# Optimization experiments

Hardware: AMD Instinct MI355X
Metric: run time of the kernel (lower is better)

## Reference

```python
import jax, jax.numpy as jnp
import numpy as np
import math

G0, G1 = 24, 24           # initial/current grid size (command(initial_grid_size=(24,24), ...))
N = G0 * G1               # 576 spatial tokens
PREFIX = 1                # num_prefix_tokens (cls token)
EPS = 0.1                 # get_eps((24,24)): 0.5*23^2/0.1^2 = 26450 <= 32500, no doubling
COEF = float(max(G0, G1) ** 2)          # 576.0, sigmoid_fn coefficient
B_SHIFT = math.log(COEF - 1.0)          # b = log(575)
CLAMP = max(-0.5 * (max(G0, G1) - 1) ** 2, -6550.0)  # -264.5


def setup_inputs() -> dict:
    key = jax.random.key(0)
    k1, k2, k3 = jax.random.split(key, 3)
    head_dim = 64
    q = jax.random.normal(k1, (8, 12, N + PREFIX, head_dim), dtype=jnp.float32)
    W_var = jax.random.normal(k2, (head_dim, 2), dtype=jnp.float32) * (head_dim ** -0.5)
    b_var = jnp.zeros((2,), dtype=jnp.float32)
    W_alpha = jax.random.normal(k3, (head_dim, 1), dtype=jnp.float32) * (head_dim ** -0.5)
    b_alpha = jnp.zeros((1,), dtype=jnp.float32)
    return {"q": q, "W_var": W_var, "b_var": b_var, "W_alpha": W_alpha, "b_alpha": b_alpha}


def _gaussian_numerator():
    # coords: (N, 2) integer grid positions
    ii, jj = jnp.meshgrid(jnp.arange(G0), jnp.arange(G1), indexing="ij")
    coords = jnp.stack([ii, jj], axis=-1).reshape(N, 2).astype(jnp.float32)
    d = -0.5 * (coords[:, None, :] - coords[None, :, :]) ** 2  # (N, N, 2)
    return jnp.maximum(d, CLAMP)


def reference(q, W_var, b_var, W_alpha, b_alpha):
    qs = q[..., PREFIX:, :]                                   # (B, H, N, C)
    # var = coef * sigmoid(linear(q) - b), shape (B, H, N, 2)
    var = COEF * jax.nn.sigmoid(jnp.einsum("bhnc,ck->bhnk", qs, W_var) + b_var - B_SHIFT)
    # alpha = softplus(linear(q)), shape (B, H, N, 1)
    alpha = jax.nn.softplus(jnp.einsum("bhnc,ck->bhnk", qs, W_alpha) + b_alpha)
    d = _gaussian_numerator()                                 # (N, N, 2)
    # broadcast divide -> sum over coord dim -> exp: (B, H, N, N)
    gaussian = jnp.exp(jnp.sum(d[None, None] / (var[:, :, :, None, :] + EPS), axis=-1))
    addition = alpha * gaussian                               # alpha broadcasts over last dim
    # pad prefix rows/cols with 0 at the beginning -> (B, H, N+1, N+1)
    return jnp.pad(addition, ((0, 0), (0, 0), (PREFIX, 0), (PREFIX, 0)))
```

## Files before the change

kernel.cpp:

```cpp
#include <hip/hip_runtime.h>
#include <math.h>

#define G 24
#define NPTS (G * G)
#define ROWS (NPTS + 1)
#define HD 64
#define BH (8 * 12)
#define EPSF 0.1f
#define COEFF 576.0f
#define BSHIFT 6.3543700408f
#define RPB 8
#define BPI ((ROWS + RPB - 1) / RPB)

typedef float f32x4 __attribute__((ext_vector_type(4)));

__global__ __launch_bounds__(256) void gaussian_augment_kernel(
    const float* __restrict__ q,
    const float* __restrict__ Wv,
    const float* __restrict__ bv,
    const float* __restrict__ Wa,
    const float* __restrict__ ba,
    float* __restrict__ out)
{
    const int bh  = blockIdx.x / BPI;
    const int blk = blockIdx.x - bh * BPI;
    const int r0  = blk * RPB;
    const int Ract = min(RPB, ROWS - r0);
    const int tid = threadIdx.x;

    __shared__ float s_dot[RPB][3];
    __shared__ float s_par[RPB][3];
    __shared__ float s_ex0[RPB][G];
    __shared__ float s_ex1[RPB][G];

    const int wave = tid >> 6;
    const int lane = tid & 63;
    #pragma unroll
    for (int pass = 0; pass < 2; ++pass) {
        const int rr = wave + 4 * pass;
        if (rr < Ract) {
            const int r = r0 + rr;
            const float* qrow = q + ((size_t)bh * ROWS + r) * HD;
            const float qv = qrow[lane];
            float p0 = qv * Wv[2 * lane + 0];
            float p1 = qv * Wv[2 * lane + 1];
            float p2 = qv * Wa[lane];
            #pragma unroll
            for (int off = 32; off >= 1; off >>= 1) {
                p0 += __shfl_xor(p0, off);
                p1 += __shfl_xor(p1, off);
                p2 += __shfl_xor(p2, off);
            }
            if (lane == 0) {
                s_dot[rr][0] = p0;
                s_dot[rr][1] = p1;
                s_dot[rr][2] = p2;
            }
        }
    }
    __syncthreads();

    if (tid < Ract) {
        const int r = r0 + tid;
        const float x0 = s_dot[tid][0] + bv[0] - BSHIFT;
        const float x1 = s_dot[tid][1] + bv[1] - BSHIFT;
        const float xa = s_dot[tid][2] + ba[0];
        const float var0 = COEFF / (1.0f + expf(-x0));
        const float var1 = COEFF / (1.0f + expf(-x1));
        s_par[tid][0] = 1.0f / (var0 + EPSF);
        s_par[tid][1] = 1.0f / (var1 + EPSF);
        const float alpha = fmaxf(xa, 0.0f) + log1pf(expf(-fabsf(xa)));
        s_par[tid][2] = (r == 0) ? 0.0f : alpha;
    }
    __syncthreads();

    for (int e = tid; e < Ract * 48; e += 256) {
        const int rr = e / 48;
        const int k  = e - rr * 48;
        const int r  = r0 + rr;
        const int n  = (r > 0) ? r - 1 : 0;
        const int in_ = n / G;
        const int jn_ = n - in_ * G;
        if (k < G) {
            const float t = (float)(in_ - k);
            s_ex0[rr][k] = s_par[rr][2] * expf(-0.5f * t * t * s_par[rr][0]);
        } else {
            const float t = (float)(jn_ - (k - G));
            s_ex1[rr][k - G] = expf(-0.5f * t * t * s_par[rr][1]);
        }
    }
    __syncthreads();

    const size_t base = ((size_t)bh * ROWS + r0) * ROWS;
    const int span  = Ract * ROWS;
    const size_t E  = base + span;
    const size_t S0 = base & ~(size_t)3;
    const int nch   = (int)((E - S0 + 3) >> 2);

    for (int idx = tid; idx < nch; idx += 256) {
        const size_t g0 = S0 + (size_t)4 * idx;
        const int e0 = (int)((long long)g0 - (long long)base);
        float v[4];
        #pragma unroll
        for (int t = 0; t < 4; ++t) {
            const int e = e0 + t;
            float val = 0.0f;
            if (e >= 0 && e < span) {
                const unsigned eu = (unsigned)e;
                const int rr = (int)(eu / 577u);
                const int c  = e - rr * 577;
                if (c > 0) {
                    const unsigned m = (unsigned)(c - 1);
                    const int im = (int)(m / 24u);
                    const int jm = (int)m - im * 24;
                    val = s_ex0[rr][im] * s_ex1[rr][jm];
                }
            }
            v[t] = val;
        }
        if (e0 >= 0 && e0 + 4 <= span) {
            f32x4 pk = { v[0], v[1], v[2], v[3] };
            __builtin_nontemporal_store(pk, (f32x4*)(out + g0));
        } else {
            #pragma unroll
            for (int t = 0; t < 4; ++t) {
                const int e = e0 + t;
                if (e >= 0 && e < span) out[g0 + t] = v[t];
            }
        }
    }
}

extern "C" void kernel_launch(void* const* d_in, const int* in_sizes, int n_in,
                              void* d_out, int out_size, void* d_ws, size_t ws_size,
                              hipStream_t stream) {
    const float* q  = (const float*)d_in[0];
    const float* Wv = (const float*)d_in[1];
    const float* bv = (const float*)d_in[2];
    const float* Wa = (const float*)d_in[3];
    const float* ba = (const float*)d_in[4];
    float* out = (float*)d_out;

    const int grid = BH * BPI;
    gaussian_augment_kernel<<<grid, 256, 0, stream>>>(q, Wv, bv, Wa, ba, out);
}
```

Before: 37.18 us.

## Assign two output rows per wavefront and drop block-level synchronisation

Work is now split per wavefront: each wave handles a pair of rows. It computes both row projections with shuffles, builds its own 96-entry exp table in shared memory, and writes the two rows. This removes the three __syncthreads barriers and the serial per-row parameter phase. It also replaces the divide by 577 with a compare. The trade-off is more per-wave redundant work, shorter store loops per wave, and no barrier between the table writes and the reads within a wave, which relies on lockstep execution inside the wave.

```diff
diff --git a/kernel.cpp b/kernel.cpp
--- a/kernel.cpp
+++ b/kernel.cpp
@@ -9,8 +9,8 @@
 #define EPSF 0.1f
 #define COEFF 576.0f
 #define BSHIFT 6.3543700408f
-#define RPB 8
-#define BPI ((ROWS + RPB - 1) / RPB)
+#define PAIRS 289
+#define WPB 4
 
 typedef float f32x4 __attribute__((ext_vector_type(4)));
 
@@ -22,102 +22,102 @@
     const float* __restrict__ ba,
     float* __restrict__ out)
 {
-    const int bh  = blockIdx.x / BPI;
-    const int blk = blockIdx.x - bh * BPI;
-    const int r0  = blk * RPB;
-    const int Ract = min(RPB, ROWS - r0);
-    const int tid = threadIdx.x;
+    const int tid  = threadIdx.x;
+    const int lane = tid & 63;
+    const int wv   = tid >> 6;
 
-    __shared__ float s_dot[RPB][3];
-    __shared__ float s_par[RPB][3];
-    __shared__ float s_ex0[RPB][G];
-    __shared__ float s_ex1[RPB][G];
+    __shared__ float s_tab[WPB][96];
 
-    const int wave = tid >> 6;
-    const int lane = tid & 63;
+    const int gw = blockIdx.x * WPB + wv;
+    const int bh = gw / PAIRS;
+    const int p  = gw - bh * PAIRS;
+    const int rA = 2 * p;
+    const bool twoRows = (rA + 1) < ROWS;
+
+    const float* qbase = q + ((size_t)bh * ROWS + rA) * HD;
+    const float qv0 = qbase[lane];
+    const float qv1 = twoRows ? qbase[HD + lane] : 0.0f;
+    const float w0 = Wv[2 * lane + 0];
+    const float w1 = Wv[2 * lane + 1];
+    const float wa = Wa[lane];
+
+    float a0 = qv0 * w0, a1 = qv0 * w1, a2 = qv0 * wa;
+    float b0 = qv1 * w0, b1 = qv1 * w1, b2 = qv1 * wa;
     #pragma unroll
-    for (int pass = 0; pass < 2; ++pass) {
-        const int rr = wave + 4 * pass;
-        if (rr < Ract) {
-            const int r = r0 + rr;
-            const float* qrow = q + ((size_t)bh * ROWS + r) * HD;
-            const float qv = qrow[lane];
-            float p0 = qv * Wv[2 * lane + 0];
-            float p1 = qv * Wv[2 * lane + 1];
-            float p2 = qv * Wa[lane];
-            #pragma unroll
-            for (int off = 32; off >= 1; off >>= 1) {
-                p0 += __shfl_xor(p0, off);
-                p1 += __shfl_xor(p1, off);
-                p2 += __shfl_xor(p2, off);
-            }
-            if (lane == 0) {
-                s_dot[rr][0] = p0;
-                s_dot[rr][1] = p1;
-                s_dot[rr][2] = p2;
-            }
-        }
+    for (int off = 32; off >= 1; off >>= 1) {
+        a0 += __shfl_xor(a0, off);
+        a1 += __shfl_xor(a1, off);
+        a2 += __shfl_xor(a2, off);
+        b0 += __shfl_xor(b0, off);
+        b1 += __shfl_xor(b1, off);
+        b2 += __shfl_xor(b2, off);
     }
-    __syncthreads();
 
-    if (tid < Ract) {
-        const int r = r0 + tid;
-        const float x0 = s_dot[tid][0] + bv[0] - BSHIFT;
-        const float x1 = s_dot[tid][1] + bv[1] - BSHIFT;
-        const float xa = s_dot[tid][2] + ba[0];
-        const float var0 = COEFF / (1.0f + expf(-x0));
-        const float var1 = COEFF / (1.0f + expf(-x1));
-        s_par[tid][0] = 1.0f / (var0 + EPSF);
-        s_par[tid][1] = 1.0f / (var1 + EPSF);
-        const float alpha = fmaxf(xa, 0.0f) + log1pf(expf(-fabsf(xa)));
-        s_par[tid][2] = (r == 0) ? 0.0f : alpha;
+    const float bv0 = bv[0], bv1 = bv[1], ba0 = ba[0];
+
+    const float varA0 = COEFF / (1.0f + expf(-(a0 + bv0 - BSHIFT)));
+    const float varA1 = COEFF / (1.0f + expf(-(a1 + bv1 - BSHIFT)));
+    const float invA0 = 1.0f / (varA0 + EPSF);
+    const float invA1 = 1.0f / (varA1 + EPSF);
+    const float xaA   = a2 + ba0;
+    float alphaA = fmaxf(xaA, 0.0f) + log1pf(expf(-fabsf(xaA)));
+    if (rA == 0) alphaA = 0.0f;
+
+    const float varB0 = COEFF / (1.0f + expf(-(b0 + bv0 - BSHIFT)));
+    const float varB1 = COEFF / (1.0f + expf(-(b1 + bv1 - BSHIFT)));
+    const float invB0 = 1.0f / (varB0 + EPSF);
+    const float invB1 = 1.0f / (varB1 + EPSF);
+    const float xaB   = b2 + ba0;
+    float alphaB = fmaxf(xaB, 0.0f) + log1pf(expf(-fabsf(xaB)));
+    if (!twoRows) alphaB = 0.0f;
+
+    const int nA = (rA > 0) ? rA - 1 : 0;
+    const int iA = nA / G, jA = nA - (nA / G) * G;
+    const int rB = rA + 1;
+    const int nB = rB - 1;
+    const int iB = nB / G, jB = nB - (nB / G) * G;
+
+    if (lane < 48) {
+        const bool isJ = lane >= 24;
+        const int  k   = isJ ? lane - 24 : lane;
+        const float tA = (float)((isJ ? jA : iA) - k);
+        const float sA = isJ ? invA1 : invA0;
+        const float mA = isJ ? 1.0f : alphaA;
+        s_tab[wv][lane] = mA * expf(-0.5f * tA * tA * sA);
+
+        const float tB = (float)((isJ ? jB : iB) - k);
+        const float sB = isJ ? invB1 : invB0;
+        const float mB = isJ ? 1.0f : alphaB;
+        s_tab[wv][48 + lane] = mB * expf(-0.5f * tB * tB * sB);
     }
-    __syncthreads();
 
-    for (int e = tid; e < Ract * 48; e += 256) {
-        const int rr = e / 48;
-        const int k  = e - rr * 48;
-        const int r  = r0 + rr;
-        const int n  = (r > 0) ? r - 1 : 0;
-        const int in_ = n / G;
-        const int jn_ = n - in_ * G;
-        if (k < G) {
-            const float t = (float)(in_ - k);
-            s_ex0[rr][k] = s_par[rr][2] * expf(-0.5f * t * t * s_par[rr][0]);
-        } else {
-            const float t = (float)(jn_ - (k - G));
-            s_ex1[rr][k - G] = expf(-0.5f * t * t * s_par[rr][1]);
-        }
-    }
-    __syncthreads();
+    const size_t base = ((size_t)bh * ROWS + rA) * ROWS;
+    const int span  = twoRows ? 2 * ROWS : ROWS;
+    const size_t S0 = base & ~(size_t)3;
+    const int   off = (int)(base - S0);
+    const int   nch = (span + off + 3) >> 2;
+    const float* tw = s_tab[wv];
 
-    const size_t base = ((size_t)bh * ROWS + r0) * ROWS;
-    const int span  = Ract * ROWS;
-    const size_t E  = base + span;
-    const size_t S0 = base & ~(size_t)3;
-    const int nch   = (int)((E - S0 + 3) >> 2);
-
-    for (int idx = tid; idx < nch; idx += 256) {
-        const size_t g0 = S0 + (size_t)4 * idx;
-        const int e0 = (int)((long long)g0 - (long long)base);
+    for (int idx = lane; idx < nch; idx += 64) {
+        const int e0 = 4 * idx - off;
         float v[4];
         #pragma unroll
         for (int t = 0; t < 4; ++t) {
             const int e = e0 + t;
             float val = 0.0f;
             if (e >= 0 && e < span) {
-                const unsigned eu = (unsigned)e;
-                const int rr = (int)(eu / 577u);
-                const int c  = e - rr * 577;
+                const int rsel = (e >= ROWS) ? 48 : 0;
+                const int c    = (e >= ROWS) ? e - ROWS : e;
                 if (c > 0) {
                     const unsigned m = (unsigned)(c - 1);
                     const int im = (int)(m / 24u);
                     const int jm = (int)m - im * 24;
-                    val = s_ex0[rr][im] * s_ex1[rr][jm];
+                    val = tw[rsel + im] * tw[rsel + 24 + jm];
                 }
             }
             v[t] = val;
         }
+        const size_t g0 = S0 + (size_t)4 * idx;
         if (e0 >= 0 && e0 + 4 <= span) {
             f32x4 pk = { v[0], v[1], v[2], v[3] };
             __builtin_nontemporal_store(pk, (f32x4*)(out + g0));
@@ -141,6 +141,6 @@
     const float* ba = (const float*)d_in[4];
     float* out = (float*)d_out;
 
-    const int grid = BH * BPI;
+    const int grid = (BH * PAIRS) / WPB;
     gaussian_augment_kernel<<<grid, 256, 0, stream>>>(q, Wv, bv, Wa, ba, out);
 }
```

Result: slower. 40.19 us (+8.1%).

## Double rows per block, vectorize projection, and fast-path store index math

Applied to the files above, without the earlier changes.

Each block now handles 16 rows instead of 8, which halves the grid and spreads the fixed per-block setup over more output. The q projection uses 16 threads per row with float4 loads and a shared-memory partial-sum reduction instead of full-wave shuffles. The store loop gets a fast path that does one division per 4-wide chunk and handles a chunk that crosses a 24-column boundary with a select between two adjacent table entries, instead of doing per-element divisions. The cost is more branches and padded tables (25 entries), and fewer blocks may lower occupancy on a kernel that is bound by the output write.

```diff
diff --git a/kernel.cpp b/kernel.cpp
--- a/kernel.cpp
+++ b/kernel.cpp
@@ -9,7 +9,7 @@
 #define EPSF 0.1f
 #define COEFF 576.0f
 #define BSHIFT 6.3543700408f
-#define RPB 8
+#define RPB 16
 #define BPI ((ROWS + RPB - 1) / RPB)
 
 typedef float f32x4 __attribute__((ext_vector_type(4)));
@@ -28,104 +28,145 @@
     const int Ract = min(RPB, ROWS - r0);
     const int tid = threadIdx.x;
 
-    __shared__ float s_dot[RPB][3];
-    __shared__ float s_par[RPB][3];
-    __shared__ float s_ex0[RPB][G];
-    __shared__ float s_ex1[RPB][G];
+    __shared__ float s_part[RPB][16][3];
+    __shared__ float s_par[RPB][4];
+    __shared__ float s_tab[RPB][2][32];
 
-    const int wave = tid >> 6;
-    const int lane = tid & 63;
-    #pragma unroll
-    for (int pass = 0; pass < 2; ++pass) {
-        const int rr = wave + 4 * pass;
-        if (rr < Ract) {
-            const int r = r0 + rr;
-            const float* qrow = q + ((size_t)bh * ROWS + r) * HD;
-            const float qv = qrow[lane];
-            float p0 = qv * Wv[2 * lane + 0];
-            float p1 = qv * Wv[2 * lane + 1];
-            float p2 = qv * Wa[lane];
+    {
+        const int r  = tid >> 4;
+        const int kk = tid & 15;
+        float p0 = 0.f, p1 = 0.f, p2 = 0.f;
+        if (r < Ract) {
+            const float* qp = q + ((size_t)bh * ROWS + r0 + r) * HD + 4 * kk;
+            const f32x4 qv = *(const f32x4*)qp;
+            const f32x4 wv0 = *(const f32x4*)(Wv + 8 * kk);
+            const f32x4 wv1 = *(const f32x4*)(Wv + 8 * kk + 4);
+            const f32x4 wav = *(const f32x4*)(Wa + 4 * kk);
+            p0 = qv[0]*wv0[0] + qv[1]*wv0[2] + qv[2]*wv1[0] + qv[3]*wv1[2];
+            p1 = qv[0]*wv0[1] + qv[1]*wv0[3] + qv[2]*wv1[1] + qv[3]*wv1[3];
+            p2 = qv[0]*wav[0] + qv[1]*wav[1] + qv[2]*wav[2] + qv[3]*wav[3];
+        }
+        s_part[r][kk][0] = p0;
+        s_part[r][kk][1] = p1;
+        s_part[r][kk][2] = p2;
+    }
+    __syncthreads();
+
+    if (tid < 3 * RPB) {
+        const int pr = tid / 3;
+        const int pp = tid - 3 * pr;
+        if (pr < Ract) {
+            float x = 0.f;
             #pragma unroll
-            for (int off = 32; off >= 1; off >>= 1) {
-                p0 += __shfl_xor(p0, off);
-                p1 += __shfl_xor(p1, off);
-                p2 += __shfl_xor(p2, off);
+            for (int k = 0; k < 16; ++k) x += s_part[pr][k][pp];
+            float o;
+            if (pp == 2) {
+                const float xa = x + ba[0];
+                float al = fmaxf(xa, 0.f) + log1pf(expf(-fabsf(xa)));
+                if (r0 + pr == 0) al = 0.f;
+                o = al;
+            } else {
+                const float xx = x + bv[pp] - BSHIFT;
+                const float var = COEFF / (1.f + expf(-xx));
+                o = 1.f / (var + EPSF);
             }
-            if (lane == 0) {
-                s_dot[rr][0] = p0;
-                s_dot[rr][1] = p1;
-                s_dot[rr][2] = p2;
-            }
+            s_par[pr][pp] = o;
         }
     }
     __syncthreads();
 
-    if (tid < Ract) {
-        const int r = r0 + tid;
-        const float x0 = s_dot[tid][0] + bv[0] - BSHIFT;
-        const float x1 = s_dot[tid][1] + bv[1] - BSHIFT;
-        const float xa = s_dot[tid][2] + ba[0];
-        const float var0 = COEFF / (1.0f + expf(-x0));
-        const float var1 = COEFF / (1.0f + expf(-x1));
-        s_par[tid][0] = 1.0f / (var0 + EPSF);
-        s_par[tid][1] = 1.0f / (var1 + EPSF);
-        const float alpha = fmaxf(xa, 0.0f) + log1pf(expf(-fabsf(xa)));
-        s_par[tid][2] = (r == 0) ? 0.0f : alpha;
-    }
-    __syncthreads();
-
-    for (int e = tid; e < Ract * 48; e += 256) {
-        const int rr = e / 48;
-        const int k  = e - rr * 48;
-        const int r  = r0 + rr;
-        const int n  = (r > 0) ? r - 1 : 0;
-        const int in_ = n / G;
-        const int jn_ = n - in_ * G;
-        if (k < G) {
+    for (int e = tid; e < 49 * Ract; e += 256) {
+        const int rr = (unsigned)e / 49u;
+        const int k  = e - 49 * rr;
+        const int rg = r0 + rr;
+        const int n  = (rg > 0) ? rg - 1 : 0;
+        const int in_ = (unsigned)n / 24u;
+        const int jn_ = n - in_ * 24;
+        if (k < 25) {
             const float t = (float)(in_ - k);
-            s_ex0[rr][k] = s_par[rr][2] * expf(-0.5f * t * t * s_par[rr][0]);
+            s_tab[rr][0][k] = s_par[rr][2] * expf(-0.5f * t * t * s_par[rr][0]);
         } else {
-            const float t = (float)(jn_ - (k - G));
-            s_ex1[rr][k - G] = expf(-0.5f * t * t * s_par[rr][1]);
+            const float t = (float)(jn_ - (k - 25));
+            s_tab[rr][1][k - 25] = expf(-0.5f * t * t * s_par[rr][1]);
         }
     }
     __syncthreads();
 
     const size_t base = ((size_t)bh * ROWS + r0) * ROWS;
     const int span  = Ract * ROWS;
-    const size_t E  = base + span;
     const size_t S0 = base & ~(size_t)3;
-    const int nch   = (int)((E - S0 + 3) >> 2);
+    const int   off = (int)(base - S0);
+    const int   nch = (span + off + 3) >> 2;
 
     for (int idx = tid; idx < nch; idx += 256) {
+        const int eb = 4 * idx - off;
         const size_t g0 = S0 + (size_t)4 * idx;
-        const int e0 = (int)((long long)g0 - (long long)base);
-        float v[4];
-        #pragma unroll
-        for (int t = 0; t < 4; ++t) {
-            const int e = e0 + t;
-            float val = 0.0f;
-            if (e >= 0 && e < span) {
-                const unsigned eu = (unsigned)e;
-                const int rr = (int)(eu / 577u);
-                const int c  = e - rr * 577;
-                if (c > 0) {
-                    const unsigned m = (unsigned)(c - 1);
-                    const int im = (int)(m / 24u);
-                    const int jm = (int)m - im * 24;
-                    val = s_ex0[rr][im] * s_ex1[rr][jm];
+        if (eb >= 0 && eb + 4 <= span) {
+            float v0, v1, v2, v3;
+            const unsigned eu = (unsigned)eb;
+            const int rr = (int)(eu / 577u);
+            const int c0 = eb - rr * 577;
+            if (c0 >= 1 && c0 <= 573) {
+                const int m0  = c0 - 1;
+                const int im0 = (unsigned)m0 / 24u;
+                const int jm0 = m0 - im0 * 24;
+                const float ea = s_tab[rr][0][im0];
+                const float eb2 = s_tab[rr][0][im0 + 1];
+                const float* t1 = s_tab[rr][1];
+                {
+                    const int j = jm0;     const bool w = j >= 24;
+                    v0 = (w ? eb2 : ea) * t1[w ? j - 24 : j];
                 }
+                {
+                    const int j = jm0 + 1; const bool w = j >= 24;
+                    v1 = (w ? eb2 : ea) * t1[w ? j - 24 : j];
+                }
+                {
+                    const int j = jm0 + 2; const bool w = j >= 24;
+                    v2 = (w ? eb2 : ea) * t1[w ? j - 24 : j];
+                }
+                {
+                    const int j = jm0 + 3; const bool w = j >= 24;
+                    v3 = (w ? eb2 : ea) * t1[w ? j - 24 : j];
+                }
+            } else {
+                float vv[4];
+                #pragma unroll
+                for (int t = 0; t < 4; ++t) {
+                    const int e = eb + t;
+                    const unsigned eu2 = (unsigned)e;
+                    const int r2 = (int)(eu2 / 577u);
+                    const int c  = e - r2 * 577;
+                    float val = 0.f;
+                    if (c > 0) {
+                        const unsigned m = (unsigned)(c - 1);
+                        const int im = (int)(m / 24u);
+                        const int jm = (int)m - im * 24;
+                        val = s_tab[r2][0][im] * s_tab[r2][1][jm];
+                    }
+                    vv[t] = val;
+                }
+                v0 = vv[0]; v1 = vv[1]; v2 = vv[2]; v3 = vv[3];
             }
-            v[t] = val;
-        }
-        if (e0 >= 0 && e0 + 4 <= span) {
-            f32x4 pk = { v[0], v[1], v[2], v[3] };
+            f32x4 pk = { v0, v1, v2, v3 };
             __builtin_nontemporal_store(pk, (f32x4*)(out + g0));
         } else {
             #pragma unroll
             for (int t = 0; t < 4; ++t) {
-                const int e = e0 + t;
-                if (e >= 0 && e < span) out[g0 + t] = v[t];
+                const int e = eb + t;
+                if (e >= 0 && e < span) {
+                    const unsigned eu2 = (unsigned)e;
+                    const int r2 = (int)(eu2 / 577u);
+                    const int c  = e - r2 * 577;
+                    float val = 0.f;
+                    if (c > 0) {
+                        const unsigned m = (unsigned)(c - 1);
+                        const int im = (int)(m / 24u);
+                        const int jm = (int)m - im * 24;
+                        val = s_tab[r2][0][im] * s_tab[r2][1][jm];
+                    }
+                    out[g0 + t] = val;
+                }
             }
         }
     }
```

Result: slower. 40.87 us (+9.9%).
